# Kernel optimization log

Measured on AMD Instinct MI355X. Metric: run time of the kernel, lower is better.

The kernel has to match this reference:

```python
import jax, jax.numpy as jnp
import numpy as np

EPS = 1e-5
BLOCK = 16

def setup_inputs() -> dict:
    key = jax.random.key(0)
    ks = jax.random.split(key, 5)
    B, S, D = 8, 4096, 1024
    G = D // BLOCK            # 64 groups
    sq = int(np.sqrt(D))      # 32
    x = jax.random.normal(ks[0], (B, S, D), dtype=jnp.float32)
    gamma = jnp.ones((D,), jnp.float32)
    beta = jnp.zeros((D,), jnp.float32)
    block_weights = 0.5 * jax.random.normal(ks[1], (G, BLOCK, BLOCK), dtype=jnp.float32)
    W_row = 0.1 * jax.random.normal(ks[2], (sq, sq), dtype=jnp.float32)
    W_col = 0.1 * jax.random.normal(ks[3], (sq, sq), dtype=jnp.float32)
    alpha = jnp.float32(0.3)
    bias = jnp.zeros((D,), jnp.float32)
    return {"x": x, "gamma": gamma, "beta": beta, "block_weights": block_weights,
            "W_row": W_row, "W_col": W_col, "alpha": alpha, "bias": bias}

def reference(x, gamma, beta, block_weights, W_row, W_col, alpha, bias):
    D = x.shape[-1]
    G, Bk, _ = block_weights.shape      # 64, 16, 16 (D == G*Bk, no pad)
    sq = W_row.shape[0]                 # 32 (D == sq*sq, no pad)
    # LayerNorm (fp32)
    mu = jnp.mean(x, axis=-1, keepdims=True)
    var = jnp.mean(jnp.square(x - mu), axis=-1, keepdims=True)
    xn = (x - mu) * jax.lax.rsqrt(var + EPS) * gamma + beta
    x_flat = xn.reshape(-1, D)          # [N, D]
    # Block-diagonal mix: [N, G, Bk] x [G, Bk, Bk]
    xg = x_flat.reshape(-1, G, Bk)
    y = jnp.einsum('ngb,gbc->ngc', xg, block_weights).reshape(-1, D)
    block_out = jnp.flip(y, axis=-1)
    # Monarch path: [N, sq, sq] @ W_col @ W_row^T
    xgrid = x_flat.reshape(-1, sq, sq)
    z = jnp.einsum('nrc,ck,sk->nrs', xgrid, W_col, W_row).reshape(-1, D)
    out = block_out + alpha * z + bias
    return out.reshape(x.shape)
```

## Files before the change

### kernel.cpp

```cpp
#include <hip/hip_runtime.h>

typedef __bf16 bf16x8 __attribute__((ext_vector_type(8)));
typedef __bf16 bf16x4 __attribute__((ext_vector_type(4)));
typedef float f32x4 __attribute__((ext_vector_type(4)));

#define EPS 1e-5f
#define TILES_PER_BLOCK 8

typedef __attribute__((address_space(3))) unsigned int lds_u32;
typedef const __attribute__((address_space(1))) unsigned int glb_u32;

__global__ __launch_bounds__(256) void hbsl_precompute(
    const float* __restrict__ bw, const float* __restrict__ W_row,
    const float* __restrict__ W_col, const float* __restrict__ alpha_p,
    __bf16* __restrict__ mt, __bf16* __restrict__ bwt)
{
    const int t = threadIdx.x;
    if (blockIdx.x == 0) {
        const float alpha = alpha_p[0];
        #pragma unroll
        for (int k = 0; k < 4; ++k) {
            int flat = t + 256 * k;
            int s = flat >> 5, c = flat & 31;
            float acc = 0.f;
            #pragma unroll 8
            for (int kk = 0; kk < 32; ++kk)
                acc += W_col[c * 32 + kk] * W_row[s * 32 + kk];
            mt[s * 32 + c] = (__bf16)(alpha * acc);
        }
    } else {
        int g = blockIdx.x - 1;
        int c = t >> 4, b = t & 15;
        bwt[g * 256 + c * 16 + b] = (__bf16)bw[g * 256 + b * 16 + c];
    }
}

__global__ __launch_bounds__(512, 2) void hbsl_main(
    const float* __restrict__ x, const float* __restrict__ gamma,
    const float* __restrict__ beta, const float* __restrict__ bias,
    const __bf16* __restrict__ mt, const __bf16* __restrict__ bwt,
    float* __restrict__ out)
{
    __shared__ float xr[2][16384];
    __shared__ float bias_s[1024];
    const int t = threadIdx.x;
    const int lane = t & 63;
    const int wv = t >> 6;
    const int q = lane >> 4, n = lane & 15;

    const bf16x8 mfrag0 = *(const bf16x8*)(mt + n * 32 + q * 8);
    const bf16x8 mfrag1 = *(const bf16x8*)(mt + (16 + n) * 32 + q * 8);
    bf16x8 bwf[4];
    #pragma unroll
    for (int p = 0; p < 4; ++p) {
        const int o0 = wv * 8 + 2 * p;
        const int gb = 31 - (o0 >> 1);
        const int g = (q >= 2) ? (2 * gb + 1) : (2 * gb);
        const int e = (q >= 2) ? (q - 2) * 8 : q * 8;
        bwf[p] = *(const bf16x8*)(bwt + g * 256 + (15 - n) * 16 + e);
    }
    *(float2*)(&bias_s[t * 2]) = *(const float2*)(bias + t * 2);

    float4 g4[8], b4[8];
    int dofs[8];
    #pragma unroll
    for (int j = 0; j < 8; ++j) {
        const int r = 2 * wv + (j >> 2);
        const int D = (((j & 3) * 64 + lane) ^ ((r & 7) << 1));
        dofs[j] = r * 1024 + D * 4;
        g4[j] = *(const float4*)(gamma + D * 4);
        b4[j] = *(const float4*)(beta + D * 4);
    }

    bf16x8 bz;
    #pragma unroll
    for (int i = 0; i < 8; ++i) bz[i] = (__bf16)0.f;

    const int nx = n & 7;
    const int nbase = (n >> 1) * 4096 + (n & 1) * 1024;

    {
        const float* xt = x + (size_t)(blockIdx.x * 16) * 1024;
        #pragma unroll
        for (int k = 0; k < 8; ++k) {
            lds_u32* lp = (lds_u32*)(&xr[0][wv * 2048 + k * 256]);
            __builtin_amdgcn_global_load_lds((glb_u32*)(xt + dofs[k]), lp, 16, 0, 0);
        }
    }
    __syncthreads();

    for (int tt = 0; tt < TILES_PER_BLOCK; ++tt) {
        const int cur = tt & 1;
        const int tile = blockIdx.x + 256 * tt;
        const int rbase = tile * 16;
        __bf16* xnb = (__bf16*)(&xr[cur][0]);

        f32x4 xg[8];
        #pragma unroll
        for (int j = 0; j < 8; ++j)
            xg[j] = *(const f32x4*)(&xr[cur][wv * 2048 + j * 256 + lane * 4]);
        float s0 = 0.f, q0 = 0.f, s1 = 0.f, q1 = 0.f;
        #pragma unroll
        for (int j = 0; j < 4; ++j) {
            s0 += xg[j][0] + xg[j][1] + xg[j][2] + xg[j][3];
            q0 += xg[j][0]*xg[j][0] + xg[j][1]*xg[j][1]
                + xg[j][2]*xg[j][2] + xg[j][3]*xg[j][3];
            s1 += xg[j+4][0] + xg[j+4][1] + xg[j+4][2] + xg[j+4][3];
            q1 += xg[j+4][0]*xg[j+4][0] + xg[j+4][1]*xg[j+4][1]
                + xg[j+4][2]*xg[j+4][2] + xg[j+4][3]*xg[j+4][3];
        }
        #pragma unroll
        for (int m = 1; m < 64; m <<= 1) {
            s0 += __shfl_xor(s0, m, 64);
            q0 += __shfl_xor(q0, m, 64);
            s1 += __shfl_xor(s1, m, 64);
            q1 += __shfl_xor(q1, m, 64);
        }
        const float mu0 = s0 * (1.f / 1024.f);
        const float rs0 = rsqrtf(q0 * (1.f / 1024.f) - mu0 * mu0 + EPS);
        const float mu1 = s1 * (1.f / 1024.f);
        const float rs1 = rsqrtf(q1 * (1.f / 1024.f) - mu1 * mu1 + EPS);
        #pragma unroll
        for (int j = 0; j < 8; ++j) {
            const float mu = (j < 4) ? mu0 : mu1;
            const float rs = (j < 4) ? rs0 : rs1;
            bf16x4 w;
            w[0] = (__bf16)((xg[j][0] - mu) * rs * g4[j].x + b4[j].x);
            w[1] = (__bf16)((xg[j][1] - mu) * rs * g4[j].y + b4[j].y);
            w[2] = (__bf16)((xg[j][2] - mu) * rs * g4[j].z + b4[j].z);
            w[3] = (__bf16)((xg[j][3] - mu) * rs * g4[j].w + b4[j].w);
            const int P = (j & 3) * 64 + lane;
            *(bf16x4*)(&xnb[wv * 4096 + (j >> 2) * 1024 + P * 4]) = w;
        }

        __syncthreads();

        if (tt + 1 < TILES_PER_BLOCK) {
            const float* xt = x + (size_t)(rbase + 256 * 16) * 1024;
            #pragma unroll
            for (int k = 0; k < 8; ++k) {
                lds_u32* lp = (lds_u32*)(&xr[cur ^ 1][wv * 2048 + k * 256]);
                __builtin_amdgcn_global_load_lds((glb_u32*)(xt + dofs[k]), lp, 16, 0, 0);
            }
        }

        float* orow = out + (size_t)(rbase + n) * 1024;
        #pragma unroll
        for (int p = 0; p < 4; ++p) {
            const int o0 = wv * 8 + 2 * p;
            const int rw = o0 >> 1;
            const int gp = 31 - rw;
            bf16x8 az = *(const bf16x8*)(&xnb[nbase + ((4 * rw + q) ^ nx) * 8]);
            bf16x8 ay = *(const bf16x8*)(&xnb[nbase + ((4 * gp + q) ^ nx) * 8]);
            bf16x8 a0 = (q >= 2) ? bwf[p] : bz;
            bf16x8 a1 = (q <  2) ? bwf[p] : bz;
            f32x4 b0 = *(const f32x4*)(&bias_s[o0 * 16 + q * 4]);
            f32x4 b1 = *(const f32x4*)(&bias_s[o0 * 16 + 16 + q * 4]);
            f32x4 d0 = __builtin_amdgcn_mfma_f32_16x16x32_bf16(mfrag0, az, b0, 0, 0, 0);
            f32x4 d1 = __builtin_amdgcn_mfma_f32_16x16x32_bf16(mfrag1, az, b1, 0, 0, 0);
            d0 = __builtin_amdgcn_mfma_f32_16x16x32_bf16(a0, ay, d0, 0, 0, 0);
            d1 = __builtin_amdgcn_mfma_f32_16x16x32_bf16(a1, ay, d1, 0, 0, 0);
            float* op = orow + o0 * 16 + q * 4;
            *(f32x4*)op        = d0;
            *(f32x4*)(op + 16) = d1;
        }

        __syncthreads();
    }
}

extern "C" void kernel_launch(void* const* d_in, const int* in_sizes, int n_in,
                              void* d_out, int out_size, void* d_ws, size_t ws_size,
                              hipStream_t stream) {
    const float* x      = (const float*)d_in[0];
    const float* gamma  = (const float*)d_in[1];
    const float* beta   = (const float*)d_in[2];
    const float* bw     = (const float*)d_in[3];
    const float* W_row  = (const float*)d_in[4];
    const float* W_col  = (const float*)d_in[5];
    const float* alpha  = (const float*)d_in[6];
    const float* bias   = (const float*)d_in[7];
    float* o = (float*)d_out;

    __bf16* mt  = (__bf16*)d_ws;
    __bf16* bwt = (__bf16*)((char*)d_ws + 2048);

    hipLaunchKernelGGL(hbsl_precompute, dim3(65), dim3(256), 0, stream,
                       bw, W_row, W_col, alpha, mt, bwt);
    hipLaunchKernelGGL(hbsl_main, dim3(256), dim3(512), 0, stream,
                       x, gamma, beta, bias, mt, bwt, o);
}
```

Measured before the change: 257.0 us.

## Restructure main loop into 4-buffer pipeline with 8-row tiles and register bias

Tiles shrink from 16 rows to 8 rows, giving 16 iterations per block, and LDS becomes four rotating buffers. Global-to-LDS DMA is issued two tiles ahead, and the stats/normalize step for the next tile overlaps the MFMA phase of the current one, so each iteration needs one barrier instead of two. Bias moves from LDS into registers and the LDS swizzle is simplified. The cost is that half of each MFMA's output rows are discarded (only n<8 is stored), which doubles MFMA work per output row, and register pressure rises.

```diff
diff --git a/kernel.cpp b/kernel.cpp
--- a/kernel.cpp
+++ b/kernel.cpp
@@ -5,7 +5,8 @@
 typedef float f32x4 __attribute__((ext_vector_type(4)));
 
 #define EPS 1e-5f
-#define TILES_PER_BLOCK 8
+#define NB 256
+#define ITERS 16
 
 typedef __attribute__((address_space(3))) unsigned int lds_u32;
 typedef const __attribute__((address_space(1))) unsigned int glb_u32;
@@ -41,16 +42,17 @@
     const __bf16* __restrict__ mt, const __bf16* __restrict__ bwt,
     float* __restrict__ out)
 {
-    __shared__ float xr[2][16384];
-    __shared__ float bias_s[1024];
+    __shared__ float xr[4][8192];
     const int t = threadIdx.x;
     const int lane = t & 63;
     const int wv = t >> 6;
     const int q = lane >> 4, n = lane & 15;
+    const int r8 = n & 7;
 
     const bf16x8 mfrag0 = *(const bf16x8*)(mt + n * 32 + q * 8);
     const bf16x8 mfrag1 = *(const bf16x8*)(mt + (16 + n) * 32 + q * 8);
     bf16x8 bwf[4];
+    f32x4 biasr[8];
     #pragma unroll
     for (int p = 0; p < 4; ++p) {
         const int o0 = wv * 8 + 2 * p;
@@ -58,114 +60,98 @@
         const int g = (q >= 2) ? (2 * gb + 1) : (2 * gb);
         const int e = (q >= 2) ? (q - 2) * 8 : q * 8;
         bwf[p] = *(const bf16x8*)(bwt + g * 256 + (15 - n) * 16 + e);
+        biasr[2 * p]     = *(const f32x4*)(bias + o0 * 16 + q * 4);
+        biasr[2 * p + 1] = *(const f32x4*)(bias + o0 * 16 + 16 + q * 4);
     }
-    *(float2*)(&bias_s[t * 2]) = *(const float2*)(bias + t * 2);
-
-    float4 g4[8], b4[8];
-    int dofs[8];
+    float4 g4[4], b4[4];
     #pragma unroll
-    for (int j = 0; j < 8; ++j) {
-        const int r = 2 * wv + (j >> 2);
-        const int D = (((j & 3) * 64 + lane) ^ ((r & 7) << 1));
-        dofs[j] = r * 1024 + D * 4;
-        g4[j] = *(const float4*)(gamma + D * 4);
-        b4[j] = *(const float4*)(beta + D * 4);
+    for (int k = 0; k < 4; ++k) {
+        g4[k] = *(const float4*)(gamma + k * 256 + lane * 4);
+        b4[k] = *(const float4*)(beta + k * 256 + lane * 4);
     }
-
     bf16x8 bz;
     #pragma unroll
     for (int i = 0; i < 8; ++i) bz[i] = (__bf16)0.f;
 
-    const int nx = n & 7;
-    const int nbase = (n >> 1) * 4096 + (n & 1) * 1024;
+    auto DMA_TILE = [&](int buf, int tile) {
+        const float* src = x + (size_t)(tile * 8 + wv) * 1024 + lane * 4;
+        #pragma unroll
+        for (int k = 0; k < 4; ++k) {
+            lds_u32* lp = (lds_u32*)(&xr[buf][wv * 1024 + k * 256]);
+            __builtin_amdgcn_global_load_lds((glb_u32*)(src + k * 256), lp, 16, 0, 0);
+        }
+    };
 
-    {
-        const float* xt = x + (size_t)(blockIdx.x * 16) * 1024;
+    auto STATS = [&](int buf) {
+        f32x4 xv[4];
         #pragma unroll
-        for (int k = 0; k < 8; ++k) {
-            lds_u32* lp = (lds_u32*)(&xr[0][wv * 2048 + k * 256]);
-            __builtin_amdgcn_global_load_lds((glb_u32*)(xt + dofs[k]), lp, 16, 0, 0);
-        }
-    }
-    __syncthreads();
-
-    for (int tt = 0; tt < TILES_PER_BLOCK; ++tt) {
-        const int cur = tt & 1;
-        const int tile = blockIdx.x + 256 * tt;
-        const int rbase = tile * 16;
-        __bf16* xnb = (__bf16*)(&xr[cur][0]);
-
-        f32x4 xg[8];
+        for (int k = 0; k < 4; ++k)
+            xv[k] = *(const f32x4*)(&xr[buf][wv * 1024 + k * 256 + lane * 4]);
+        float s = 0.f, ss = 0.f;
         #pragma unroll
-        for (int j = 0; j < 8; ++j)
-            xg[j] = *(const f32x4*)(&xr[cur][wv * 2048 + j * 256 + lane * 4]);
-        float s0 = 0.f, q0 = 0.f, s1 = 0.f, q1 = 0.f;
-        #pragma unroll
-        for (int j = 0; j < 4; ++j) {
-            s0 += xg[j][0] + xg[j][1] + xg[j][2] + xg[j][3];
-            q0 += xg[j][0]*xg[j][0] + xg[j][1]*xg[j][1]
-                + xg[j][2]*xg[j][2] + xg[j][3]*xg[j][3];
-            s1 += xg[j+4][0] + xg[j+4][1] + xg[j+4][2] + xg[j+4][3];
-            q1 += xg[j+4][0]*xg[j+4][0] + xg[j+4][1]*xg[j+4][1]
-                + xg[j+4][2]*xg[j+4][2] + xg[j+4][3]*xg[j+4][3];
+        for (int k = 0; k < 4; ++k) {
+            s  += xv[k][0] + xv[k][1] + xv[k][2] + xv[k][3];
+            ss += xv[k][0]*xv[k][0] + xv[k][1]*xv[k][1]
+                + xv[k][2]*xv[k][2] + xv[k][3]*xv[k][3];
         }
         #pragma unroll
         for (int m = 1; m < 64; m <<= 1) {
-            s0 += __shfl_xor(s0, m, 64);
-            q0 += __shfl_xor(q0, m, 64);
-            s1 += __shfl_xor(s1, m, 64);
-            q1 += __shfl_xor(q1, m, 64);
+            s  += __shfl_xor(s, m, 64);
+            ss += __shfl_xor(ss, m, 64);
         }
-        const float mu0 = s0 * (1.f / 1024.f);
-        const float rs0 = rsqrtf(q0 * (1.f / 1024.f) - mu0 * mu0 + EPS);
-        const float mu1 = s1 * (1.f / 1024.f);
-        const float rs1 = rsqrtf(q1 * (1.f / 1024.f) - mu1 * mu1 + EPS);
+        const float mu = s * (1.f / 1024.f);
+        const float rs = rsqrtf(ss * (1.f / 1024.f) - mu * mu + EPS);
+        __bf16* xnb = (__bf16*)(&xr[buf][0]);
         #pragma unroll
-        for (int j = 0; j < 8; ++j) {
-            const float mu = (j < 4) ? mu0 : mu1;
-            const float rs = (j < 4) ? rs0 : rs1;
+        for (int k = 0; k < 4; ++k) {
             bf16x4 w;
-            w[0] = (__bf16)((xg[j][0] - mu) * rs * g4[j].x + b4[j].x);
-            w[1] = (__bf16)((xg[j][1] - mu) * rs * g4[j].y + b4[j].y);
-            w[2] = (__bf16)((xg[j][2] - mu) * rs * g4[j].z + b4[j].z);
-            w[3] = (__bf16)((xg[j][3] - mu) * rs * g4[j].w + b4[j].w);
-            const int P = (j & 3) * 64 + lane;
-            *(bf16x4*)(&xnb[wv * 4096 + (j >> 2) * 1024 + P * 4]) = w;
+            w[0] = (__bf16)((xv[k][0] - mu) * rs * g4[k].x + b4[k].x);
+            w[1] = (__bf16)((xv[k][1] - mu) * rs * g4[k].y + b4[k].y);
+            w[2] = (__bf16)((xv[k][2] - mu) * rs * g4[k].z + b4[k].z);
+            w[3] = (__bf16)((xv[k][3] - mu) * rs * g4[k].w + b4[k].w);
+            const int c = (k * 256 + lane * 4) ^ (wv << 3);
+            *(bf16x4*)(&xnb[wv * 2048 + c]) = w;
         }
+    };
 
-        __syncthreads();
-
-        if (tt + 1 < TILES_PER_BLOCK) {
-            const float* xt = x + (size_t)(rbase + 256 * 16) * 1024;
-            #pragma unroll
-            for (int k = 0; k < 8; ++k) {
-                lds_u32* lp = (lds_u32*)(&xr[cur ^ 1][wv * 2048 + k * 256]);
-                __builtin_amdgcn_global_load_lds((glb_u32*)(xt + dofs[k]), lp, 16, 0, 0);
-            }
-        }
-
-        float* orow = out + (size_t)(rbase + n) * 1024;
+    auto MFMA_PHASE = [&](int buf, int tile) {
+        const __bf16* xnb = (const __bf16*)(&xr[buf][0]);
+        float* orow = out + (size_t)(tile * 8 + n) * 1024;
         #pragma unroll
         for (int p = 0; p < 4; ++p) {
             const int o0 = wv * 8 + 2 * p;
             const int rw = o0 >> 1;
             const int gp = 31 - rw;
-            bf16x8 az = *(const bf16x8*)(&xnb[nbase + ((4 * rw + q) ^ nx) * 8]);
-            bf16x8 ay = *(const bf16x8*)(&xnb[nbase + ((4 * gp + q) ^ nx) * 8]);
+            bf16x8 az = *(const bf16x8*)(&xnb[r8 * 2048 + ((rw * 32 + q * 8) ^ (r8 << 3))]);
+            bf16x8 ay = *(const bf16x8*)(&xnb[r8 * 2048 + ((gp * 32 + q * 8) ^ (r8 << 3))]);
             bf16x8 a0 = (q >= 2) ? bwf[p] : bz;
             bf16x8 a1 = (q <  2) ? bwf[p] : bz;
-            f32x4 b0 = *(const f32x4*)(&bias_s[o0 * 16 + q * 4]);
-            f32x4 b1 = *(const f32x4*)(&bias_s[o0 * 16 + 16 + q * 4]);
-            f32x4 d0 = __builtin_amdgcn_mfma_f32_16x16x32_bf16(mfrag0, az, b0, 0, 0, 0);
-            f32x4 d1 = __builtin_amdgcn_mfma_f32_16x16x32_bf16(mfrag1, az, b1, 0, 0, 0);
+            f32x4 d0 = __builtin_amdgcn_mfma_f32_16x16x32_bf16(mfrag0, az, biasr[2*p], 0, 0, 0);
+            f32x4 d1 = __builtin_amdgcn_mfma_f32_16x16x32_bf16(mfrag1, az, biasr[2*p+1], 0, 0, 0);
             d0 = __builtin_amdgcn_mfma_f32_16x16x32_bf16(a0, ay, d0, 0, 0, 0);
             d1 = __builtin_amdgcn_mfma_f32_16x16x32_bf16(a1, ay, d1, 0, 0, 0);
-            float* op = orow + o0 * 16 + q * 4;
-            *(f32x4*)op        = d0;
-            *(f32x4*)(op + 16) = d1;
+            if (n < 8) {
+                float* op = orow + o0 * 16 + q * 4;
+                *(f32x4*)op        = d0;
+                *(f32x4*)(op + 16) = d1;
+            }
         }
+    };
 
-        __syncthreads();
+    const int tb = blockIdx.x;
+
+    DMA_TILE(0, tb);
+    DMA_TILE(1, tb + NB);
+    __syncthreads();
+    STATS(0);
+    __syncthreads();
+
+    #pragma unroll
+    for (int i = 0; i < ITERS; ++i) {
+        if (i + 2 < ITERS) DMA_TILE((i + 2) & 3, tb + NB * (i + 2));
+        if (i + 1 < ITERS) STATS((i + 1) & 3);
+        MFMA_PHASE(i & 3, tb + NB * i);
+        if (i + 1 < ITERS) __syncthreads();
     }
 }
 
@@ -187,6 +173,6 @@
 
     hipLaunchKernelGGL(hbsl_precompute, dim3(65), dim3(256), 0, stream,
                        bw, W_row, W_col, alpha, mt, bwt);
-    hipLaunchKernelGGL(hbsl_main, dim3(256), dim3(512), 0, stream,
+    hipLaunchKernelGGL(hbsl_main, dim3(NB), dim3(512), 0, stream,
                        x, gamma, beta, bias, mt, bwt, o);
 }
```

New measurement: 254.3 us. No clear change (-1.1%).
